# Kernel optimization log

Measured on AMD Instinct MI355X. Metric: run time of the kernel, lower is better.

The kernel has to match this reference:

```python
import jax, jax.numpy as jnp
import numpy as np
from jax import lax

# Fixed image shape (H, W) for all images, standard detection resize
H_IMG, W_IMG = 800.0, 1333.0
SCORE_THRESH = 0.05
NMS_THRESH = 0.5
DET_PER_IMG = 100
K_PRE = 2048  # NMS candidate budget per image (after score threshold)
BBOX_XFORM_CLIP = float(np.log(1000.0 / 16.0))
WX, WY, WW, WH = 10.0, 10.0, 5.0, 5.0  # bbox_reg_weights


def setup_inputs() -> dict:
    B, P, C = 8, 2000, 81
    key = jax.random.key(0)
    k1, k2, k3, k4 = jax.random.split(key, 4)
    class_logits = 2.0 * jax.random.normal(k1, (B * P, C), jnp.float32)
    box_regression = 0.5 * jax.random.normal(k2, (B * P, C * 4), jnp.float32)
    # valid proposal boxes inside the image: (x1,y1) + (w,h)
    xy = jax.random.uniform(k3, (B, P, 2), jnp.float32) * jnp.array([W_IMG - 128.0, H_IMG - 128.0], jnp.float32)
    wh = 1.0 + 127.0 * jax.random.uniform(k4, (B, P, 2), jnp.float32)
    proposals = jnp.concatenate([xy, xy + wh], axis=-1)
    return {"class_logits": class_logits, "box_regression": box_regression, "proposals": proposals}


def _decode(rel, boxes):
    # BoxCoder.decode: rel [N, C, 4], boxes [N, 4] -> [N, C, 4]
    w = boxes[:, 2] - boxes[:, 0]
    h = boxes[:, 3] - boxes[:, 1]
    cx = boxes[:, 0] + 0.5 * w
    cy = boxes[:, 1] + 0.5 * h
    dx = rel[..., 0] / WX
    dy = rel[..., 1] / WY
    dw = jnp.minimum(rel[..., 2] / WW, BBOX_XFORM_CLIP)
    dh = jnp.minimum(rel[..., 3] / WH, BBOX_XFORM_CLIP)
    pcx = dx * w[:, None] + cx[:, None]
    pcy = dy * h[:, None] + cy[:, None]
    pw = jnp.exp(dw) * w[:, None]
    ph = jnp.exp(dh) * h[:, None]
    return jnp.stack([pcx - 0.5 * pw, pcy - 0.5 * ph, pcx + 0.5 * pw, pcy + 0.5 * ph], axis=-1)


def _pairwise_iou(b):
    # b: [K, 4] -> [K, K]
    area = jnp.maximum(b[:, 2] - b[:, 0], 0.0) * jnp.maximum(b[:, 3] - b[:, 1], 0.0)
    lt = jnp.maximum(b[:, None, :2], b[None, :, :2])
    rb = jnp.minimum(b[:, None, 2:], b[None, :, 2:])
    wh = jnp.maximum(rb - lt, 0.0)
    inter = wh[..., 0] * wh[..., 1]
    union = area[:, None] + area[None, :] - inter
    return inter / jnp.maximum(union, 1e-9)


def _greedy_nms(boxes, valid):
    # boxes: [K, 4] sorted by score desc; valid: [K] bool. Exact greedy NMS.
    K = boxes.shape[0]
    iou = _pairwise_iou(boxes)
    idx = jnp.arange(K)

    def body(i, keep):
        sup = keep[i] & (iou[i] > NMS_THRESH) & (idx > i)
        return keep & ~sup

    return lax.fori_loop(0, K, body, valid)


def reference(class_logits, box_regression, proposals):
    B, P, _ = proposals.shape
    C = class_logits.shape[-1]
    # decode all class-specific boxes, softmax scores
    rel = box_regression.reshape(-1, C, 4)
    pred = _decode(rel, proposals.reshape(-1, 4)).reshape(B, P, C, 4)
    scores = jax.nn.softmax(class_logits, axis=-1).reshape(B, P, C)
    # drop background class 0
    M = P * (C - 1)
    boxes = pred[:, :, 1:, :].reshape(B, M, 4)
    scores = scores[:, :, 1:].reshape(B, M)
    labels = jnp.broadcast_to(jnp.arange(1, C)[None, None, :], (B, P, C - 1)).reshape(B, M)
    # clip to image
    x1 = jnp.clip(boxes[..., 0], 0.0, W_IMG)
    y1 = jnp.clip(boxes[..., 1], 0.0, H_IMG)
    x2 = jnp.clip(boxes[..., 2], 0.0, W_IMG)
    y2 = jnp.clip(boxes[..., 3], 0.0, H_IMG)
    boxes = jnp.stack([x1, y1, x2, y2], axis=-1)
    # score threshold + remove_small_boxes(min_size=0.01), as a validity mask
    valid = (scores > SCORE_THRESH) & ((x2 - x1) >= 0.01) & ((y2 - y1) >= 0.01)
    masked = jnp.where(valid, scores, -1.0)
    # top-K candidates per image (sorted desc -> NMS visiting order)
    top_s, top_i = lax.top_k(masked, K_PRE)
    top_b = jnp.take_along_axis(boxes, top_i[..., None], axis=1)
    top_l = jnp.take_along_axis(labels, top_i, axis=1)
    top_v = top_s > 0.0
    # batched_nms: per-class coordinate offsets so classes never overlap
    off = top_l.astype(jnp.float32) * (jnp.maximum(W_IMG, H_IMG) + 1.0)
    keep = jax.vmap(_greedy_nms)(top_b + off[..., None], top_v)
    final = jnp.where(keep, top_s, -1.0)
    det_s, det_i = lax.top_k(final, DET_PER_IMG)
    det_b = jnp.take_along_axis(top_b, det_i[..., None], axis=1)
    det_l = jnp.take_along_axis(top_l, det_i, axis=1)
    det_valid = det_s > 0.0  # padding slots have score -1
    return det_b, det_s, det_l, det_valid
```

## Files before the change

### kernel.cpp

```cpp
#include <hip/hip_runtime.h>
#include <cstdint>
#include <cstddef>

typedef unsigned long long u64;

constexpr int Bn   = 8;
constexpr int Pn   = 2000;
constexpr int Cn   = 81;
constexpr int CM1  = 80;
constexpr int KPRE = 2048;
constexpr int NDET = 100;
constexpr int SECP = 8;
constexpr int NSEC2 = Pn / SECP;
constexpr int SSLOT = 160;
constexpr int NSEG = 4;
constexpr int RUNL = 2048;
constexpr int K2CAP = 4096;
constexpr float W_IMG = 1333.0f;
constexpr float H_IMG = 800.0f;
constexpr float XFORM_CLIP = 4.135166556742356f;
constexpr float NMS_OFF = 1334.0f;

constexpr size_t OFF_SL   = 0;
constexpr size_t OFF_SC   = (size_t)Bn * NSEC2 * SSLOT * 8;
constexpr size_t OFF_RUNS = OFF_SC + (size_t)Bn * NSEC2 * 4;

__device__ __forceinline__ void decode_clip(const float4 rv, float w, float h,
                                            float cx, float cy, float out[4]) {
  float dx = rv.x / 10.0f;
  float dy = rv.y / 10.0f;
  float dw = fminf(rv.z / 5.0f, XFORM_CLIP);
  float dh = fminf(rv.w / 5.0f, XFORM_CLIP);
  float pcx = dx * w + cx;
  float pcy = dy * h + cy;
  float pw = expf(dw) * w;
  float ph = expf(dh) * h;
  out[0] = fminf(fmaxf(pcx - 0.5f * pw, 0.0f), W_IMG);
  out[1] = fminf(fmaxf(pcy - 0.5f * ph, 0.0f), H_IMG);
  out[2] = fminf(fmaxf(pcx + 0.5f * pw, 0.0f), W_IMG);
  out[3] = fminf(fmaxf(pcy + 0.5f * ph, 0.0f), H_IMG);
}

__device__ __forceinline__ void key_decode(u64 key, int b,
                                           const float* __restrict__ reg,
                                           const float* __restrict__ props,
                                           float bx[4], int& label, float& sc) {
  sc = __uint_as_float((unsigned)(key >> 32));
  bx[0] = bx[1] = bx[2] = bx[3] = 0.0f;
  label = 0;
  if (key != 0ull) {
    int m = (int)(0xFFFFFFFFu - (unsigned)key);
    int p = m / CM1;
    int c = m - p * CM1 + 1;
    int nidx = b * Pn + p;
    const float4 pb = *reinterpret_cast<const float4*>(props + (size_t)nidx * 4);
    float w = pb.z - pb.x, h = pb.w - pb.y;
    float cx = pb.x + 0.5f * w, cy = pb.y + 0.5f * h;
    float4 rv = *reinterpret_cast<const float4*>(reg + (size_t)nidx * (Cn * 4) + c * 4);
    decode_clip(rv, w, h, cx, cy, bx);
    label = c;
  }
}

__global__ __launch_bounds__(512) void
k1_score(const float* __restrict__ logits, const float* __restrict__ reg,
         const float* __restrict__ props, u64* __restrict__ slices,
         int* __restrict__ scnt) {
  int blk = blockIdx.x, t = threadIdx.x, lane = t & 63, wv = t >> 6;
  int b = blk / NSEC2, sec = blk % NSEC2;
  __shared__ u64 cbuf[SSLOT];
  __shared__ int cnt_sh;
  if (t == 0) cnt_sh = 0;
  __syncthreads();

  {
    int p = sec * SECP + wv;
    int wid = b * Pn + p;
    const float* lg = logits + (size_t)wid * Cn;
    float x0 = lg[lane];
    float x1 = (lane < Cn - 64) ? lg[64 + lane] : -3.4e38f;
    float mx = fmaxf(x0, x1);
    for (int m = 32; m; m >>= 1) mx = fmaxf(mx, __shfl_xor(mx, m, 64));
    float e0 = expf(x0 - mx);
    float e1 = (lane < Cn - 64) ? expf(x1 - mx) : 0.0f;
    float ssum = e0 + e1;
    for (int m = 32; m; m >>= 1) ssum += __shfl_xor(ssum, m, 64);

    const float4 pb = *reinterpret_cast<const float4*>(props + (size_t)wid * 4);
    float w = pb.z - pb.x, h = pb.w - pb.y;
    float cx = pb.x + 0.5f * w, cy = pb.y + 0.5f * h;
    const float* rrow = reg + (size_t)wid * (Cn * 4);

    u64 key0 = 0ull, key1 = 0ull;
    if (lane >= 1) {
      float sc = e0 / ssum;
      if (sc > 0.05f) {
        float4 rv = *reinterpret_cast<const float4*>(rrow + lane * 4);
        float bx[4];
        decode_clip(rv, w, h, cx, cy, bx);
        if ((bx[2] - bx[0] >= 0.01f) && (bx[3] - bx[1] >= 0.01f)) {
          unsigned m = (unsigned)(p * CM1 + (lane - 1));
          key0 = ((u64)__float_as_uint(sc) << 32) | (0xFFFFFFFFu - m);
        }
      }
    }
    if (lane < Cn - 64) {
      int c = 64 + lane;
      float sc = e1 / ssum;
      if (sc > 0.05f) {
        float4 rv = *reinterpret_cast<const float4*>(rrow + c * 4);
        float bx[4];
        decode_clip(rv, w, h, cx, cy, bx);
        if ((bx[2] - bx[0] >= 0.01f) && (bx[3] - bx[1] >= 0.01f)) {
          unsigned m = (unsigned)(p * CM1 + (c - 1));
          key1 = ((u64)__float_as_uint(sc) << 32) | (0xFFFFFFFFu - m);
        }
      }
    }
    u64 bal0 = __ballot(key0 != 0ull);
    u64 bal1 = __ballot(key1 != 0ull);
    int tot = __popcll(bal0) + __popcll(bal1);
    if (tot) {
      int base = 0;
      if (lane == 0) base = atomicAdd(&cnt_sh, tot);
      base = __shfl(base, 0, 64);
      int r0 = __popcll(bal0 & ((1ull << lane) - 1ull));
      int r1 = __popcll(bal0) + __popcll(bal1 & ((1ull << lane) - 1ull));
      if (key0) cbuf[base + r0] = key0;
      if (key1) cbuf[base + r1] = key1;
    }
  }
  __syncthreads();
  int n = cnt_sh;
  for (int i = t; i < n; i += 512) slices[(size_t)blk * SSLOT + i] = cbuf[i];
  if (t == 0) scnt[blk] = n;
}

template <int CHV>
__device__ __forceinline__ void mp_round(u64* buf, int base, int nA, int nB,
                                         int outLen, int tid) {
  const u64* A = buf + base;
  const u64* B = buf + base + nA;
  int d = tid * CHV;
  u64 rg[CHV];
  int cnt = 0;
  if (d < outLen) {
    int lo = max(0, d - nB), hi = min(d, nA);
    while (lo < hi) {
      int mid = (lo + hi) >> 1;
      if (A[mid] >= B[d - 1 - mid]) lo = mid + 1; else hi = mid;
    }
    int i = lo, j = d - lo;
    for (int e = 0; e < CHV && d + e < outLen; e++) {
      u64 v;
      if (j >= nB || (i < nA && A[i] >= B[j])) v = A[i++];
      else v = B[j++];
      rg[cnt++] = v;
    }
  }
  __syncthreads();
  for (int e = 0; e < cnt; e++) buf[base + d + e] = rg[e];
  __syncthreads();
}

template <int CHV>
__device__ __forceinline__ void mp_seg_round(u64* buf, int len, int cnt, int t) {
  int tps = len / CHV;
  int seg = t / tps;
  int tid = t - seg * tps;
  int base = seg * len;
  bool act = (base < cnt);
  int nA = len >> 1;
  int d = tid * CHV;
  u64 rg[CHV];
  if (act) {
    const u64* A = buf + base;
    const u64* B = buf + base + nA;
    int lo = max(0, d - nA), hi = min(d, nA);
    while (lo < hi) {
      int mid = (lo + hi) >> 1;
      if (A[mid] >= B[d - 1 - mid]) lo = mid + 1; else hi = mid;
    }
    int i = lo, j = d - lo;
    #pragma unroll
    for (int e = 0; e < CHV; e++) {
      u64 v;
      if (j >= nA || (i < nA && A[i] >= B[j])) v = A[i++];
      else v = B[j++];
      rg[e] = v;
    }
  }
  __syncthreads();
  if (act) {
    #pragma unroll
    for (int e = 0; e < CHV; e++) buf[base + d + e] = rg[e];
  }
  __syncthreads();
}

__device__ __forceinline__ void append_chunk(u64 key, bool valid, u64* buf,
                                             int* cnt_sh, int lane) {
  u64 bal = __ballot(valid);
  int tot = __popcll(bal);
  if (tot) {
    int base = 0;
    if (lane == 0) base = atomicAdd(cnt_sh, tot);
    base = __shfl(base, 0, 64);
    int rank = __popcll(bal & ((1ull << lane) - 1ull));
    int pos = base + rank;
    if (valid && pos < K2CAP) buf[pos] = key;
  }
}

__global__ __launch_bounds__(1024) void
k2b_sort(const u64* __restrict__ slices, const int* __restrict__ scnt,
         u64* __restrict__ runs) {
  int blk = blockIdx.x, t = threadIdx.x, lane = t & 63, w = t >> 6;
  int b = blk >> 2, seg = blk & 3;
  int s0 = seg * 62 + min(seg, 2);
  int ns = 62 + (seg < 2 ? 1 : 0);
  __shared__ u64 buf[K2CAP];
  __shared__ int lcnt2[63];
  __shared__ int cnt_sh;
  if (t == 0) cnt_sh = 0;
  if (t < ns) lcnt2[t] = scnt[b * NSEC2 + s0 + t];
  __syncthreads();

  {
    int sl = w;
    int n0 = 0; u64 kv = 0ull;
    if (sl < ns) {
      n0 = lcnt2[sl];
      if (lane < n0) kv = slices[(size_t)(b * NSEC2 + s0 + sl) * SSLOT + lane];
    }
    while (sl < ns) {
      int nx = sl + 16;
      int n1 = 0; u64 kn = 0ull;
      if (nx < ns) {
        n1 = lcnt2[nx];
        if (lane < n1)
          kn = slices[(size_t)(b * NSEC2 + s0 + nx) * SSLOT + lane];
      }
      append_chunk(kv, (lane < n0) && (kv != 0ull), buf, &cnt_sh, lane);
      for (int i0 = 64; i0 < n0; i0 += 64) {
        int i = i0 + lane;
        u64 ke = (i < n0) ? slices[(size_t)(b * NSEC2 + s0 + sl) * SSLOT + i]
                          : 0ull;
        append_chunk(ke, ke != 0ull, buf, &cnt_sh, lane);
      }
      sl = nx; n0 = n1; kv = kn;
    }
  }
  __syncthreads();
  int cnt = min(cnt_sh, K2CAP);
  for (int i = cnt + t; i < K2CAP; i += 1024) buf[i] = 0ull;
  __syncthreads();

  for (int r = w; (r << 6) < cnt; r += 16) {
    u64 v = buf[(r << 6) | lane];
    #pragma unroll
    for (int k = 2; k <= 64; k <<= 1) {
      #pragma unroll
      for (int j = k >> 1; j > 0; j >>= 1) {
        u64 o = __shfl_xor(v, j, 64);
        bool dir = ((lane & k) == 0);
        bool lower = ((lane & j) == 0);
        u64 mn = (v < o) ? v : o;
        u64 mx = (v < o) ? o : v;
        v = (dir == lower) ? mx : mn;
      }
    }
    buf[(r << 6) | lane] = v;
  }
  __syncthreads();

  if (cnt > 64)   mp_seg_round<4>(buf, 128, cnt, t);
  if (cnt > 128)  mp_seg_round<4>(buf, 256, cnt, t);
  if (cnt > 256)  mp_seg_round<4>(buf, 512, cnt, t);
  if (cnt > 512)  mp_seg_round<4>(buf, 1024, cnt, t);
  if (cnt > 1024) mp_seg_round<4>(buf, 2048, cnt, t);
  if (cnt > 2048) mp_round<2>(buf, 0, 2048, 2048, 2048, t);

  for (int i = t; i < RUNL; i += 1024)
    runs[(size_t)blk * RUNL + i] = buf[i];
}

__global__ __launch_bounds__(1024) void
k3_nms(const u64* __restrict__ runs, const float* __restrict__ reg,
       const float* __restrict__ props, float* __restrict__ out) {
  int b = blockIdx.x, t = threadIdx.x, lane = t & 63, w = t >> 6;
  __shared__ u64 bufS[NSEG * RUNL];
  __shared__ u64 bufD[NSEG * RUNL];
  __shared__ u64 maskb[256][4];
  __shared__ u64 keepw[KPRE / 64];
  __shared__ int accI[NDET];
  __shared__ int kcnt_sh;
  float4* obox = (float4*)bufD;

  for (int i = t; i < NSEG * RUNL; i += 1024)
    bufS[i] = runs[(size_t)b * NSEG * RUNL + i];
  __syncthreads();

  #pragma unroll
  for (int p = 0; p < 2; p++) {
    const u64* A = bufS + p * 4096;
    const u64* B = A + 2048;
    int d = t * 4;
    int lo = max(0, d - 2048), hi = min(d, 2048);
    while (lo < hi) {
      int mid = (lo + hi) >> 1;
      if (A[mid] >= B[d - 1 - mid]) lo = mid + 1; else hi = mid;
    }
    int i = lo, j = d - lo;
    #pragma unroll
    for (int e = 0; e < 4; e++) {
      u64 v;
      if (j >= 2048 || (i < 2048 && A[i] >= B[j])) v = A[i++];
      else v = B[j++];
      bufD[p * 4096 + d + e] = v;
    }
  }
  __syncthreads();
  {
    const u64* A = bufD;
    const u64* B = bufD + 4096;
    int d = t * 2;
    int lo = max(0, d - 4096), hi = min(d, 4096);
    while (lo < hi) {
      int mid = (lo + hi) >> 1;
      if (A[mid] >= B[d - 1 - mid]) lo = mid + 1; else hi = mid;
    }
    int i = lo, j = d - lo;
    #pragma unroll
    for (int e = 0; e < 2; e++) {
      u64 v;
      if (j >= 4096 || (i < 4096 && A[i] >= B[j])) v = A[i++];
      else v = B[j++];
      bufS[d + e] = v;
    }
  }
  __syncthreads();

  u64 k0 = bufS[t], k1v = bufS[t + 1024];
  {
    u64 bal = __ballot(k0 != 0ull);
    if (lane == 0) keepw[w] = bal;
    bal = __ballot(k1v != 0ull);
    if (lane == 0) keepw[16 + w] = bal;
  }
  __syncthreads();
  #pragma unroll
  for (int s = 0; s < 2; s++) {
    int j = t + s * 1024;
    u64 key = s ? k1v : k0;
    float bx[4]; int label; float sc;
    key_decode(key, b, reg, props, bx, label, sc);
    float off = (float)label * NMS_OFF;
    obox[j] = make_float4(bx[0] + off, bx[1] + off, bx[2] + off, bx[3] + off);
  }
  __syncthreads();

  int kcount = 0;
  for (int w0 = 0; w0 < KPRE && kcount < NDET; w0 += 256) {
    if (w0 > 0 && kcount > 0) {
      if (t < 256) {
        int j = w0 + t;
        u64 kwv = keepw[j >> 6];
        bool alive = (kwv >> (j & 63)) & 1ull;
        if (alive) {
          float4 jb = obox[j];
          float jar = fmaxf(jb.z - jb.x, 0.0f) * fmaxf(jb.w - jb.y, 0.0f);
          for (int a = 0; a < kcount; a++) {
            float4 ab = obox[accI[a]];
            float ix1 = fmaxf(ab.x, jb.x), iy1 = fmaxf(ab.y, jb.y);
            float ix2 = fminf(ab.z, jb.z), iy2 = fminf(ab.w, jb.w);
            float iw = fmaxf(ix2 - ix1, 0.0f), ih = fmaxf(iy2 - iy1, 0.0f);
            float inter = iw * ih;
            if (inter > 0.0f) {
              float aar = fmaxf(ab.z - ab.x, 0.0f) * fmaxf(ab.w - ab.y, 0.0f);
              float iou = inter / fmaxf(aar + jar - inter, 1e-9f);
              if (iou > 0.5f) { alive = false; break; }
            }
          }
        }
        u64 bal = __ballot(alive);
        if (lane == 0) keepw[(w0 >> 6) + (t >> 6)] = bal;
      }
      __syncthreads();
    }
    {
      int r = t >> 2, wd = t & 3;
      int rgp = w0 + r;
      bool ralive = (keepw[rgp >> 6] >> (rgp & 63)) & 1ull;
      float4 rb = obox[rgp];
      float rar = fmaxf(rb.z - rb.x, 0.0f) * fmaxf(rb.w - rb.y, 0.0f);
      u64 m = 0;
      if (ralive) {
        int cb0 = w0 + wd * 64;
        for (int jj = 0; jj < 64; jj++) {
          int cg = cb0 + jj;
          float4 cb = obox[cg];
          float ix1 = fmaxf(rb.x, cb.x), iy1 = fmaxf(rb.y, cb.y);
          float ix2 = fminf(rb.z, cb.z), iy2 = fminf(rb.w, cb.w);
          float iw = fmaxf(ix2 - ix1, 0.0f), ih = fmaxf(iy2 - iy1, 0.0f);
          float inter = iw * ih;
          if (inter > 0.0f && cg > rgp) {
            float car = fmaxf(cb.z - cb.x, 0.0f) * fmaxf(cb.w - cb.y, 0.0f);
            float iou = inter / fmaxf(rar + car - inter, 1e-9f);
            if (iou > 0.5f) m |= (1ull << jj);
          }
        }
      }
      maskb[r][wd] = m;
    }
    __syncthreads();
    if (w == 0) {
      u64 kw0 = keepw[(w0 >> 6) + 0];
      u64 kw1 = keepw[(w0 >> 6) + 1];
      u64 kw2 = keepw[(w0 >> 6) + 2];
      u64 kw3 = keepw[(w0 >> 6) + 3];
      int kc = kcount;
      #pragma unroll
      for (int wq = 0; wq < 4; wq++) {
        u64 cw = (wq == 0) ? kw0 : (wq == 1) ? kw1 : (wq == 2) ? kw2 : kw3;
        if (cw == 0ull) continue;
        for (int rb0 = 0; rb0 < 64 && kc < NDET; rb0 += 4) {
          u64 gbits = (cw >> rb0) & 0xFull;
          int r = wq * 64 + rb0;
          u64 rm0a = maskb[r][0],   rm0b = maskb[r][1],   rm0c = maskb[r][2],   rm0d = maskb[r][3];
          u64 rm1a = maskb[r+1][0], rm1b = maskb[r+1][1], rm1c = maskb[r+1][2], rm1d = maskb[r+1][3];
          u64 rm2a = maskb[r+2][0], rm2b = maskb[r+2][1], rm2c = maskb[r+2][2], rm2d = maskb[r+2][3];
          u64 rm3a = maskb[r+3][0], rm3b = maskb[r+3][1], rm3c = maskb[r+3][2], rm3d = maskb[r+3][3];
          if (gbits == 0ull) continue;
          #pragma unroll
          for (int d = 0; d < 4; d++) {
            u64 cwq = (wq == 0) ? kw0 : (wq == 1) ? kw1 : (wq == 2) ? kw2 : kw3;
            if ((cwq >> (rb0 + d)) & 1ull) {
              if (lane == 0) accI[kc] = w0 + r + d;
              kc++;
              if (kc >= NDET) break;
              u64 ma = (d == 0) ? rm0a : (d == 1) ? rm1a : (d == 2) ? rm2a : rm3a;
              u64 mb = (d == 0) ? rm0b : (d == 1) ? rm1b : (d == 2) ? rm2b : rm3b;
              u64 mc = (d == 0) ? rm0c : (d == 1) ? rm1c : (d == 2) ? rm2c : rm3c;
              u64 md = (d == 0) ? rm0d : (d == 1) ? rm1d : (d == 2) ? rm2d : rm3d;
              kw0 &= ~ma; kw1 &= ~mb; kw2 &= ~mc; kw3 &= ~md;
            }
          }
          cw = (wq == 0) ? kw0 : (wq == 1) ? kw1 : (wq == 2) ? kw2 : kw3;
        }
      }
      if (lane == 0) {
        keepw[(w0 >> 6) + 0] = kw0;
        keepw[(w0 >> 6) + 1] = kw1;
        keepw[(w0 >> 6) + 2] = kw2;
        keepw[(w0 >> 6) + 3] = kw3;
        kcnt_sh = kc;
      }
    }
    __syncthreads();
    kcount = kcnt_sh;
  }

  if (t == 0 && kcount < NDET) {
    int run = kcount;
    for (int wq = 0; wq < KPRE / 64 && run < NDET; wq++) {
      u64 nk = ~keepw[wq];
      while (nk && run < NDET) {
        int bit2 = __ffsll((long long)nk) - 1;
        nk &= nk - 1;
        accI[run++] = wq * 64 + bit2;
      }
    }
  }
  __syncthreads();

  if (t < NDET) {
    int k = accI[t];
    bool kept = t < kcount;
    u64 key = bufS[k];
    float bx[4]; int label; float sc;
    key_decode(key, b, reg, props, bx, label, sc);
    int oi = b * NDET + t;
    out[(size_t)oi * 4 + 0] = bx[0];
    out[(size_t)oi * 4 + 1] = bx[1];
    out[(size_t)oi * 4 + 2] = bx[2];
    out[(size_t)oi * 4 + 3] = bx[3];
    out[Bn * NDET * 4 + oi] = kept ? sc : -1.0f;
    out[Bn * NDET * 5 + oi] = (float)label;
    out[Bn * NDET * 6 + oi] = kept ? 1.0f : 0.0f;
  }
}

extern "C" void kernel_launch(void* const* d_in, const int* in_sizes, int n_in,
                              void* d_out, int out_size, void* d_ws, size_t ws_size,
                              hipStream_t stream) {
  const float* logits = (const float*)d_in[0];
  const float* reg    = (const float*)d_in[1];
  const float* props  = (const float*)d_in[2];
  float* out = (float*)d_out;
  char* ws = (char*)d_ws;

  u64* slices = (u64*)(ws + OFF_SL);
  int* scnt   = (int*)(ws + OFF_SC);
  u64* runs   = (u64*)(ws + OFF_RUNS);

  k1_score<<<Bn * NSEC2, 512, 0, stream>>>(logits, reg, props, slices, scnt);
  k2b_sort<<<Bn * NSEG, 1024, 0, stream>>>(slices, scnt, runs);
  k3_nms<<<Bn, 1024, 0, stream>>>(runs, reg, props, out);
}
```

Before: 127.0 us.

## Fuse sort and NMS kernels with last-block-done atomic counter

Merges the per-segment sort kernel and the per-image NMS kernel into one launch. Each sort block writes its run, fences, and increments a per-image counter; the last of the four blocks for an image then performs the merge and NMS. This removes one kernel launch and its inter-kernel gap. In exchange, every block now reserves the larger NMS shared memory, which may reduce co-residency of the sort blocks, and the NMS tail still runs on only one block per image.

After: 142.7 us. 1.12x slower.

```diff
diff --git a/kernel.cpp b/kernel.cpp
--- a/kernel.cpp
+++ b/kernel.cpp
@@ -24,6 +24,7 @@
 constexpr size_t OFF_SL   = 0;
 constexpr size_t OFF_SC   = (size_t)Bn * NSEC2 * SSLOT * 8;
 constexpr size_t OFF_RUNS = OFF_SC + (size_t)Bn * NSEC2 * 4;
+constexpr size_t OFF_DONE = OFF_RUNS + (size_t)Bn * NSEG * RUNL * 8;
 
 __device__ __forceinline__ void decode_clip(const float4 rv, float w, float h,
                                             float cx, float cy, float out[4]) {
@@ -65,12 +66,13 @@
 __global__ __launch_bounds__(512) void
 k1_score(const float* __restrict__ logits, const float* __restrict__ reg,
          const float* __restrict__ props, u64* __restrict__ slices,
-         int* __restrict__ scnt) {
+         int* __restrict__ scnt, int* __restrict__ done) {
   int blk = blockIdx.x, t = threadIdx.x, lane = t & 63, wv = t >> 6;
   int b = blk / NSEC2, sec = blk % NSEC2;
   __shared__ u64 cbuf[SSLOT];
   __shared__ int cnt_sh;
   if (t == 0) cnt_sh = 0;
+  if (blk < Bn && t == 0) done[blk] = 0;
   __syncthreads();
 
   {
@@ -213,15 +215,24 @@
 }
 
 __global__ __launch_bounds__(1024) void
-k2b_sort(const u64* __restrict__ slices, const int* __restrict__ scnt,
-         u64* __restrict__ runs) {
+k2_sortnms(const u64* __restrict__ slices, const int* __restrict__ scnt,
+           u64* __restrict__ runs, int* __restrict__ done,
+           const float* __restrict__ reg, const float* __restrict__ props,
+           float* __restrict__ out) {
   int blk = blockIdx.x, t = threadIdx.x, lane = t & 63, w = t >> 6;
   int b = blk >> 2, seg = blk & 3;
+  __shared__ u64 bufS[NSEG * RUNL];
+  __shared__ u64 bufD[NSEG * RUNL];
+  __shared__ u64 maskb[256][4];
+  __shared__ u64 keepw[KPRE / 64];
+  __shared__ int accI[NDET];
+  __shared__ int lcnt2[63];
+  __shared__ int cnt_sh, kcnt_sh, old_sh;
+  u64* buf = bufS;
+  float4* obox = (float4*)bufD;
+
   int s0 = seg * 62 + min(seg, 2);
   int ns = 62 + (seg < 2 ? 1 : 0);
-  __shared__ u64 buf[K2CAP];
-  __shared__ int lcnt2[63];
-  __shared__ int cnt_sh;
   if (t == 0) cnt_sh = 0;
   if (t < ns) lcnt2[t] = scnt[b * NSEC2 + s0 + t];
   __syncthreads();
@@ -283,19 +294,12 @@
 
   for (int i = t; i < RUNL; i += 1024)
     runs[(size_t)blk * RUNL + i] = buf[i];
-}
-
-__global__ __launch_bounds__(1024) void
-k3_nms(const u64* __restrict__ runs, const float* __restrict__ reg,
-       const float* __restrict__ props, float* __restrict__ out) {
-  int b = blockIdx.x, t = threadIdx.x, lane = t & 63, w = t >> 6;
-  __shared__ u64 bufS[NSEG * RUNL];
-  __shared__ u64 bufD[NSEG * RUNL];
-  __shared__ u64 maskb[256][4];
-  __shared__ u64 keepw[KPRE / 64];
-  __shared__ int accI[NDET];
-  __shared__ int kcnt_sh;
-  float4* obox = (float4*)bufD;
+
+  __threadfence();
+  if (t == 0) old_sh = atomicAdd(&done[b], 1);
+  __syncthreads();
+  if ((old_sh & 3) != 3) return;
+  __threadfence();
 
   for (int i = t; i < NSEG * RUNL; i += 1024)
     bufS[i] = runs[(size_t)b * NSEG * RUNL + i];
@@ -503,8 +507,9 @@
   u64* slices = (u64*)(ws + OFF_SL);
   int* scnt   = (int*)(ws + OFF_SC);
   u64* runs   = (u64*)(ws + OFF_RUNS);
-
-  k1_score<<<Bn * NSEC2, 512, 0, stream>>>(logits, reg, props, slices, scnt);
-  k2b_sort<<<Bn * NSEG, 1024, 0, stream>>>(slices, scnt, runs);
-  k3_nms<<<Bn, 1024, 0, stream>>>(runs, reg, props, out);
-}
+  int* done   = (int*)(ws + OFF_DONE);
+
+  k1_score<<<Bn * NSEC2, 512, 0, stream>>>(logits, reg, props, slices, scnt, done);
+  k2_sortnms<<<Bn * NSEG, 1024, 0, stream>>>(slices, scnt, runs, done,
+                                             reg, props, out);
+}
```
